# Kernel tuning notes

Hardware: AMD Instinct MI355X
Metric: run time of the kernel (lower is better)

The kernel has to match this reference:

```python
import jax, jax.numpy as jnp
import numpy as np

HID = 128
NEG = 9000000000000000.0  # 9e15 additive mask constant from the source


def setup_inputs() -> dict:
    key = jax.random.key(0)
    ks = jax.random.split(key, 20)
    B, N, OBS, N1, N2 = 32, 2048, 256, 8, 8
    x = jax.random.normal(ks[0], (B, N, OBS), dtype=jnp.float32)
    mask = jax.random.randint(ks[1], (B, N, N), 0, 2).astype(jnp.float32)

    def lin(kw, kb, fan_in, fan_out):
        bound = 1.0 / np.sqrt(fan_in)
        W = jax.random.uniform(kw, (fan_in, fan_out), jnp.float32, -bound, bound)
        b = jax.random.uniform(kb, (fan_out,), jnp.float32, -bound, bound)
        return W, b

    Wv, bv = lin(ks[2], ks[3], OBS, HID)
    Wk, bk = lin(ks[4], ks[5], OBS, HID)
    Wq, bq = lin(ks[6], ks[7], OBS, HID)
    Wout, bout = lin(ks[8], ks[9], HID, HID)
    Wval, bval = lin(ks[10], ks[11], HID, 1)
    Wadv1, badv1 = lin(ks[12], ks[13], HID, N1)
    Wadv2, badv2 = lin(ks[14], ks[15], HID, N2)
    return {
        'x': x, 'mask': mask,
        'Wv': Wv, 'bv': bv, 'Wk': Wk, 'bk': bk, 'Wq': Wq, 'bq': bq,
        'Wout': Wout, 'bout': bout, 'Wval': Wval, 'bval': bval,
        'Wadv1': Wadv1, 'badv1': badv1, 'Wadv2': Wadv2, 'badv2': badv2,
    }


def reference(x, mask, Wv, bv, Wk, bk, Wq, bq, Wout, bout,
              Wval, bval, Wadv1, badv1, Wadv2, badv2):
    # AttenModel
    v = jax.nn.relu(x @ Wv + bv)          # [B,N,H]
    q = jax.nn.relu(x @ Wq + bq)          # [B,N,H]
    k = jax.nn.relu(x @ Wk + bk)          # [B,N,H]
    scores = jnp.einsum('bnh,bmh->bnm', q, k)          # [B,N,N]
    scores = scores * mask - NEG * (1.0 - mask)
    att = jax.nn.softmax(scores, axis=2)
    out = jnp.einsum('bnm,bmh->bnh', att, v)            # [B,N,H]
    out = jax.nn.relu(out @ Wout + bout)                # [B,N,H]
    # Dueling heads (batch > 1, so squeeze(0) is a no-op)
    value = out @ Wval + bval                            # [B,N,1]
    adv1 = out @ Wadv1 + badv1                           # [B,N,n1]
    adv2 = out @ Wadv2 + badv2                           # [B,N,n2]
    q1 = value + adv1 - adv1.mean(axis=1, keepdims=True)
    q2 = value + adv2 - adv2.mean(axis=1, keepdims=True)
    return (q1, q2)
```

## Files before the change

kernel.cpp:

```cpp
#include <hip/hip_runtime.h>
#include <hip/hip_bf16.h>


typedef __attribute__((ext_vector_type(4))) float f32x4;
typedef __attribute__((ext_vector_type(8))) short bf16x8;
typedef __attribute__((ext_vector_type(4))) unsigned int u32x4;

#define LOG2E 1.44269504088896340736f
#define NEGC 9.0e15f

static __device__ __forceinline__ unsigned short f2bf(float f) {
  unsigned int x = __builtin_bit_cast(unsigned int, f);
  unsigned int r = (x + 0x7fffu + ((x >> 16) & 1u)) >> 16;
  return (unsigned short)r;
}
static __device__ __forceinline__ float bf2f(unsigned short u) {
  return __builtin_bit_cast(float, ((unsigned int)u) << 16);
}
static __device__ __forceinline__ unsigned int cvt_pk_bf16(float lo, float hi) {
  unsigned int r;
  asm("v_cvt_pk_bf16_f32 %0, %1, %2" : "=v"(r) : "v"(lo), "v"(hi));
  return r;
}
static __device__ __forceinline__ f32x4 mfma16(bf16x8 a, bf16x8 b, f32x4 c) {
  return __builtin_amdgcn_mfma_f32_16x16x32_bf16(a, b, c, 0, 0, 0);
}

__global__ __launch_bounds__(256) void prepack_kernel(
    const float* __restrict__ mask, unsigned long long* __restrict__ bits,
    const float* __restrict__ Wv, const float* __restrict__ Wk,
    const float* __restrict__ Wq, const float* __restrict__ Wout,
    unsigned short* __restrict__ Wf_hi, unsigned short* __restrict__ Wf_lo,
    unsigned short* __restrict__ WoutT) {
  if (blockIdx.x >= 2048) {
    int gid = (blockIdx.x - 2048) * 256 + threadIdx.x;
    if (gid < 12288) {
      int kc = gid / 1536;
      int rem = gid - kc * 1536;
      int t = rem >> 6, lane = rem & 63;
      int hf = lane & 15, qf = lane >> 4;
      int sec = t >> 3;
      int j = (t & 7) * 16 + hf;
      const float* W = (sec == 0) ? Wq : (sec == 1) ? Wk : Wv;
#pragma unroll
      for (int e = 0; e < 8; ++e) {
        int k = kc * 32 + qf * 8 + e;
        float w = W[k * 128 + j];
        unsigned short hi = f2bf(w);
        Wf_hi[gid * 8 + e] = hi;
        Wf_lo[gid * 8 + e] = f2bf(w - bf2f(hi));
      }
    } else if (gid < 12288 + 16384) {
      int i2 = gid - 12288;
      int j = i2 >> 7, c = i2 & 127;
      WoutT[i2] = f2bf(Wout[c * 128 + j]);
    }
    return;
  }
  const int lane = threadIdx.x & 63;
  const int gwave = (blockIdx.x << 2) | (threadIdx.x >> 6);
  const int T = lane & 3;
  const int sh = T << 4;
  for (int r = 0; r < 8; ++r) {
    const long row = (long)gwave * 8 + r;
    const float* mp = mask + row * 2048;
    unsigned long long* op = bits + row * 32;
#pragma unroll
    for (int g = 0; g < 8; ++g) {
      f32x4 v = *(const f32x4*)(mp + g * 256 + lane * 4);
      unsigned long long b0 = __ballot(v[0] != 0.0f);
      unsigned long long b1 = __ballot(v[1] != 0.0f);
      unsigned long long b2 = __ballot(v[2] != 0.0f);
      unsigned long long b3 = __ballot(v[3] != 0.0f);
      unsigned long long f0 = (b0 >> sh) & 0xFFFFull;
      unsigned long long f1 = (b1 >> sh) & 0xFFFFull;
      unsigned long long f2 = (b2 >> sh) & 0xFFFFull;
      unsigned long long f3 = (b3 >> sh) & 0xFFFFull;
      unsigned long long val = f0 | (f1 << 16) | (f2 << 32) | (f3 << 48);
      if (lane < 4) op[g * 4 + T] = val;
    }
  }
}

__global__ __launch_bounds__(256, 2) void proj_kernel(
    const float* __restrict__ x,
    const unsigned short* __restrict__ Wf_hi, const unsigned short* __restrict__ Wf_lo,
    const float* __restrict__ bq, const float* __restrict__ bk, const float* __restrict__ bv,
    unsigned short* __restrict__ q_bf, unsigned short* __restrict__ Kf,
    unsigned short* __restrict__ Vf) {
  __shared__ bf16x8 wst_hi[1536];
  __shared__ bf16x8 wst_lo[1536];
  __shared__ unsigned short vbuf[9216];

  const int tid = threadIdx.x;
  const int lane = tid & 63, wid = tid >> 6;
  const long rbase = (long)blockIdx.x * 64;
  const int qq = lane >> 4, hh = lane & 15;
  const long rowA = rbase + wid * 16 + hh;
  const f32x4 zero4 = {0.f, 0.f, 0.f, 0.f};
  f32x4 acc[24];
#pragma unroll
  for (int t = 0; t < 24; ++t) acc[t] = zero4;

  for (int kc = 0; kc < 8; ++kc) {
    __syncthreads();
#pragma unroll
    for (int i = 0; i < 6; ++i) {
      int idx = i * 256 + tid;
      wst_hi[idx] = *(const bf16x8*)(Wf_hi + ((long)kc * 1536 + idx) * 8);
      wst_lo[idx] = *(const bf16x8*)(Wf_lo + ((long)kc * 1536 + idx) * 8);
    }
    __syncthreads();

    const float* xp = x + rowA * 256 + kc * 32 + qq * 8;
    f32x4 x0 = *(const f32x4*)xp;
    f32x4 x1 = *(const f32x4*)(xp + 4);
    bf16x8 ah, al;
#pragma unroll
    for (int j = 0; j < 8; ++j) {
      float f = (j < 4) ? x0[j] : x1[j - 4];
      unsigned short h = f2bf(f);
      ah[j] = (short)h;
      al[j] = (short)f2bf(f - bf2f(h));
    }
#pragma unroll
    for (int t = 0; t < 24; ++t) {
      bf16x8 bh = wst_hi[t * 64 + lane];
      bf16x8 bl = wst_lo[t * 64 + lane];
      acc[t] = mfma16(ah, bh, acc[t]);
      acc[t] = mfma16(al, bh, acc[t]);
      acc[t] = mfma16(ah, bl, acc[t]);
    }
  }

  const int rowL = wid * 16 + qq * 4;
  const int b = (int)(rbase >> 11);
  const int tbase = (int)((rbase & 2047) >> 6);

  for (int sec = 0; sec < 3; ++sec) {
    __syncthreads();
#pragma unroll
    for (int tp = 0; tp < 8; ++tp) {
      const int t = sec * 8 + tp;
      const int j = tp * 16 + hh;
      const float bias = (sec == 0) ? bq[j] : (sec == 1) ? bk[j] : bv[j];
#pragma unroll
      for (int r = 0; r < 4; ++r) {
        unsigned short h = f2bf(fmaxf(acc[t][r] + bias, 0.f));
        if (sec == 2) vbuf[j * 72 + rowL + r] = h;
        else          vbuf[(rowL + r) * 136 + j] = h;
      }
    }
    __syncthreads();
    if (sec == 0) {
      const int row = tid >> 2, ch = tid & 3;
      bf16x8 w1 = *(const bf16x8*)&vbuf[row * 136 + ch * 32];
      bf16x8 w2 = *(const bf16x8*)&vbuf[row * 136 + ch * 32 + 8];
      bf16x8 w3 = *(const bf16x8*)&vbuf[row * 136 + ch * 32 + 16];
      bf16x8 w4 = *(const bf16x8*)&vbuf[row * 136 + ch * 32 + 24];
      unsigned short* op = q_bf + (rbase + row) * 128 + ch * 32;
      *(bf16x8*)op = w1;
      *(bf16x8*)(op + 8) = w2;
      *(bf16x8*)(op + 16) = w3;
      *(bf16x8*)(op + 24) = w4;
    } else if (sec == 1) {
#pragma unroll
      for (int it = 0; it < 4; ++it) {
        int gid = it * 256 + tid;
        int seg = gid >> 6, ln = gid & 63;
        int m = seg >> 2, kc = seg & 3;
        int hf = ln & 15, qf = ln >> 4;
        bf16x8 w = *(const bf16x8*)&vbuf[(m * 16 + hf) * 136 + kc * 32 + qf * 8];
        long off = (((long)(b * 32 + tbase) * 16 + seg) * 64 + ln) * 8;
        *(bf16x8*)(Kf + off) = w;
      }
    } else {
#pragma unroll
      for (int it = 0; it < 4; ++it) {
        int gid = it * 256 + tid;
        int seg = gid >> 6, ln = gid & 63;
        int ht = seg >> 1, c = seg & 1;
        int hf = ln & 15, qf = ln >> 4;
        bf16x8 w = *(const bf16x8*)&vbuf[(ht * 16 + hf) * 72 + c * 32 + qf * 8];
        long off = (((long)(b * 32 + tbase) * 16 + seg) * 64 + ln) * 8;
        *(bf16x8*)(Vf + off) = w;
      }
    }
  }
}

__global__ __launch_bounds__(256, 2) void attn_kernel(
    const unsigned short* __restrict__ q_bf, const unsigned short* __restrict__ Kf,
    const unsigned short* __restrict__ Vf,
    const unsigned long long* __restrict__ bits, unsigned short* __restrict__ out_att) {
  __shared__ bf16x8 kls[2][1024];
  __shared__ bf16x8 vls[2][1024];

  const int tid = threadIdx.x;
  const int lane = tid & 63, wid = tid >> 6;
  const int qq = lane >> 4, hh = lane & 15;
  const int orig = blockIdx.x;
  const int b = ((orig & 7) << 2) | ((orig >> 3) & 3);
  const int nb = orig >> 5;
  const long qbase = (long)b * 2048 + nb * 128 + wid * 32;

  const f32x4 zero4 = {0.f, 0.f, 0.f, 0.f};

  bf16x8 qh[2][4];
#pragma unroll
  for (int ctq = 0; ctq < 2; ++ctq)
#pragma unroll
    for (int kc = 0; kc < 4; ++kc)
      qh[ctq][kc] = *(const bf16x8*)(q_bf + (qbase + ctq * 16 + hh) * 128 + kc * 32 + qq * 8);

  const unsigned long long* br0 = bits + (qbase + hh) * 32;
  const unsigned long long* br1 = bits + (qbase + 16 + hh) * 32;
  const unsigned short* kf0 = Kf + (long)(b * 32) * 8192;
  const unsigned short* vf0 = Vf + (long)(b * 32) * 8192;

  f32x4 o_acc[8][2];
#pragma unroll
  for (int ht = 0; ht < 8; ++ht) { o_acc[ht][0] = zero4; o_acc[ht][1] = zero4; }
  float m_run[2] = {-3.0e38f, -3.0e38f};
  float l_run[2] = {0.f, 0.f};

  bf16x8 stg[8];
  const int seg0 = wid * 8;
  auto LOADREG = [&](int t) {
#pragma unroll
    for (int i = 0; i < 8; ++i) {
      int seg = seg0 + i;
      const unsigned short* src = (seg < 16)
          ? kf0 + (long)t * 8192 + (seg * 64 + lane) * 8
          : vf0 + (long)t * 8192 + ((seg - 16) * 64 + lane) * 8;
      stg[i] = *(const bf16x8*)src;
    }
  };
  auto WRITEBUF = [&](int nb2) {
#pragma unroll
    for (int i = 0; i < 8; ++i) {
      int seg = seg0 + i;
      if (seg < 16) kls[nb2][seg * 64 + lane] = stg[i];
      else          vls[nb2][(seg - 16) * 64 + lane] = stg[i];
    }
  };

  LOADREG(0);
  WRITEBUF(0);
  LOADREG(1);
  __syncthreads();

  unsigned long long bc0 = br0[0];
  unsigned long long bc1 = br1[0];
  int cur = 0;

  for (int t = 0; t < 32; ++t) {
    unsigned long long bn0 = 0, bn1 = 0;
    if (t + 1 < 32) { bn0 = br0[t + 1]; bn1 = br1[t + 1]; }

    if (t + 1 < 32) WRITEBUF(cur ^ 1);
    if (t + 2 < 32) LOADREG(t + 2);

    f32x4 s[2][4];
#pragma unroll
    for (int m = 0; m < 4; ++m) { s[0][m] = zero4; s[1][m] = zero4; }
    __builtin_amdgcn_s_setprio(1);
#pragma unroll
    for (int m = 0; m < 4; ++m) {
      bf16x8 khf[4];
#pragma unroll
      for (int kc = 0; kc < 4; ++kc) khf[kc] = kls[cur][(m * 4 + kc) * 64 + lane];
#pragma unroll
      for (int kc = 0; kc < 4; ++kc)
#pragma unroll
        for (int ctq = 0; ctq < 2; ++ctq)
          s[ctq][m] = mfma16(khf[kc], qh[ctq][kc], s[ctq][m]);
    }
    __builtin_amdgcn_s_setprio(0);

    {
      const unsigned long long bb0 = bc0 >> qq;
      const unsigned long long bb1 = bc1 >> qq;
#pragma unroll
      for (int m = 0; m < 4; ++m)
#pragma unroll
        for (int r = 0; r < 4; ++r) {
          const int sh = r * 16 + m * 4;
          s[0][m][r] = ((bb0 >> sh) & 1ull) ? s[0][m][r] : -NEGC;
          s[1][m][r] = ((bb1 >> sh) & 1ull) ? s[1][m][r] : -NEGC;
        }
    }

    unsigned int pk[2][4][2];
#pragma unroll
    for (int ctq = 0; ctq < 2; ++ctq) {
      float mx = s[ctq][0][0];
#pragma unroll
      for (int m = 0; m < 4; ++m)
#pragma unroll
        for (int r = 0; r < 4; ++r) mx = fmaxf(mx, s[ctq][m][r]);
      mx = fmaxf(mx, __shfl_xor(mx, 16, 64));
      mx = fmaxf(mx, __shfl_xor(mx, 32, 64));
      if (__any(mx > m_run[ctq] + 8.0f)) {
        float mnew = fmaxf(m_run[ctq], mx);
        float sc = exp2f((m_run[ctq] - mnew) * LOG2E);
        m_run[ctq] = mnew;
        l_run[ctq] *= sc;
#pragma unroll
        for (int ht = 0; ht < 8; ++ht) o_acc[ht][ctq] *= sc;
      }
      float ps = 0.f;
#pragma unroll
      for (int m = 0; m < 4; ++m)
#pragma unroll
        for (int r = 0; r < 4; ++r) {
          float p = exp2f((s[ctq][m][r] - m_run[ctq]) * LOG2E);
          s[ctq][m][r] = p;
          ps += p;
        }
      ps += __shfl_xor(ps, 16, 64);
      ps += __shfl_xor(ps, 32, 64);
      l_run[ctq] += ps;
#pragma unroll
      for (int m = 0; m < 4; ++m) {
        pk[ctq][m][0] = cvt_pk_bf16(s[ctq][m][0], s[ctq][m][1]);
        pk[ctq][m][1] = cvt_pk_bf16(s[ctq][m][2], s[ctq][m][3]);
      }
    }

    bf16x8 pb[2][2];
#pragma unroll
    for (int ctq = 0; ctq < 2; ++ctq)
#pragma unroll
      for (int c = 0; c < 2; ++c) {
        unsigned int a  = pk[ctq][2 * c][0];
        unsigned int bb = pk[ctq][2 * c][1];
        unsigned int cc = pk[ctq][2 * c + 1][0];
        unsigned int d  = pk[ctq][2 * c + 1][1];
        asm("v_permlane32_swap_b32 %0, %1" : "+v"(a),  "+v"(cc));
        asm("v_permlane32_swap_b32 %0, %1" : "+v"(bb), "+v"(d));
        asm("v_permlane16_swap_b32 %0, %1" : "+v"(a),  "+v"(cc));
        asm("v_permlane16_swap_b32 %0, %1" : "+v"(bb), "+v"(d));
        u32x4 w;
        w[0] = a; w[1] = bb; w[2] = cc; w[3] = d;
        pb[ctq][c] = __builtin_bit_cast(bf16x8, w);
      }

    __builtin_amdgcn_s_setprio(1);
#pragma unroll
    for (int ht = 0; ht < 8; ++ht)
#pragma unroll
      for (int c = 0; c < 2; ++c) {
        bf16x8 vf = vls[cur][(ht * 2 + c) * 64 + lane];
#pragma unroll
        for (int ctq = 0; ctq < 2; ++ctq)
          o_acc[ht][ctq] = mfma16(vf, pb[ctq][c], o_acc[ht][ctq]);
      }
    __builtin_amdgcn_s_setprio(0);

    __syncthreads();
    cur ^= 1;
    bc0 = bn0;
    bc1 = bn1;
  }

#pragma unroll
  for (int ctq = 0; ctq < 2; ++ctq) {
    float inv = 1.0f / l_run[ctq];
    const long row = qbase + ctq * 16 + hh;
#pragma unroll
    for (int ht = 0; ht < 8; ++ht) {
      f32x4 o = o_acc[ht][ctq];
      uint2 w;
      w.x = cvt_pk_bf16(o[0] * inv, o[1] * inv);
      w.y = cvt_pk_bf16(o[2] * inv, o[3] * inv);
      *(uint2*)(out_att + row * 128 + ht * 16 + qq * 4) = w;
    }
  }
}

__global__ __launch_bounds__(256) void wout_heads_kernel(
    const unsigned short* __restrict__ out_att, const unsigned short* __restrict__ WoutT,
    const float* __restrict__ bout,
    const float* __restrict__ Wval, const float* __restrict__ bval,
    const float* __restrict__ Wadv1, const float* __restrict__ badv1,
    const float* __restrict__ Wadv2, const float* __restrict__ badv2,
    float* __restrict__ value, float* __restrict__ adv1, float* __restrict__ adv2) {
  const int lane = threadIdx.x & 63, wid = threadIdx.x >> 6;
  const int qq = lane >> 4, hh = lane & 15;
  const long rowA = (long)blockIdx.x * 64 + wid * 16 + hh;
  const f32x4 zero4 = {0.f, 0.f, 0.f, 0.f};
  f32x4 acc[8];
#pragma unroll
  for (int t = 0; t < 8; ++t) acc[t] = zero4;
#pragma unroll
  for (int kc = 0; kc < 4; ++kc) {
    bf16x8 af = *(const bf16x8*)(out_att + rowA * 128 + kc * 32 + qq * 8);
#pragma unroll
    for (int t = 0; t < 8; ++t) {
      bf16x8 bf = *(const bf16x8*)(WoutT + (t * 16 + hh) * 128 + kc * 32 + qq * 8);
      acc[t] = mfma16(af, bf, acc[t]);
    }
  }
  float pv[4] = {0.f, 0.f, 0.f, 0.f};
  float pa1[4][8], pa2[4][8];
#pragma unroll
  for (int r = 0; r < 4; ++r)
#pragma unroll
    for (int j = 0; j < 8; ++j) { pa1[r][j] = 0.f; pa2[r][j] = 0.f; }
#pragma unroll
  for (int t = 0; t < 8; ++t) {
    const int col = t * 16 + hh;
    const float bo = bout[col];
    const float wv = Wval[col];
    const f32x4 w1a = *(const f32x4*)(Wadv1 + col * 8);
    const f32x4 w1b = *(const f32x4*)(Wadv1 + col * 8 + 4);
    const f32x4 w2a = *(const f32x4*)(Wadv2 + col * 8);
    const f32x4 w2b = *(const f32x4*)(Wadv2 + col * 8 + 4);
#pragma unroll
    for (int r = 0; r < 4; ++r) {
      float h = fmaxf(acc[t][r] + bo, 0.f);
      pv[r] += h * wv;
#pragma unroll
      for (int j = 0; j < 4; ++j) {
        pa1[r][j]     += h * w1a[j];
        pa1[r][4 + j] += h * w1b[j];
        pa2[r][j]     += h * w2a[j];
        pa2[r][4 + j] += h * w2b[j];
      }
    }
  }
#pragma unroll
  for (int r = 0; r < 4; ++r) {
#pragma unroll
    for (int s = 1; s < 16; s <<= 1) {
      pv[r] += __shfl_xor(pv[r], s, 64);
#pragma unroll
      for (int j = 0; j < 8; ++j) {
        pa1[r][j] += __shfl_xor(pa1[r][j], s, 64);
        pa2[r][j] += __shfl_xor(pa2[r][j], s, 64);
      }
    }
  }
  if (hh == 0) {
    const float bv0 = bval[0];
#pragma unroll
    for (int r = 0; r < 4; ++r) {
      const long row = (long)blockIdx.x * 64 + wid * 16 + qq * 4 + r;
      value[row] = pv[r] + bv0;
#pragma unroll
      for (int j = 0; j < 8; ++j) {
        adv1[row * 8 + j] = pa1[r][j] + badv1[j];
        adv2[row * 8 + j] = pa2[r][j] + badv2[j];
      }
    }
  }
}

__global__ __launch_bounds__(256) void combine_kernel(
    const float* __restrict__ value, const float* __restrict__ adv1,
    const float* __restrict__ adv2, float* __restrict__ out) {
  const int b = blockIdx.x >> 3;
  const int slice = blockIdx.x & 7;
  const int tid = threadIdx.x;
  __shared__ float red[4][16];

  float p[16];
#pragma unroll
  for (int j = 0; j < 16; ++j) p[j] = 0.f;
  for (int n = tid; n < 2048; n += 256) {
    const long row = (long)b * 2048 + n;
    const f32x4 a1a = *(const f32x4*)(adv1 + row * 8);
    const f32x4 a1b = *(const f32x4*)(adv1 + row * 8 + 4);
    const f32x4 a2a = *(const f32x4*)(adv2 + row * 8);
    const f32x4 a2b = *(const f32x4*)(adv2 + row * 8 + 4);
#pragma unroll
    for (int j = 0; j < 4; ++j) {
      p[j] += a1a[j]; p[4 + j] += a1b[j];
      p[8 + j] += a2a[j]; p[12 + j] += a2b[j];
    }
  }
#pragma unroll
  for (int s = 1; s < 64; s <<= 1)
#pragma unroll
    for (int j = 0; j < 16; ++j) p[j] += __shfl_xor(p[j], s, 64);
  const int wid = tid >> 6;
  if ((tid & 63) == 0)
#pragma unroll
    for (int j = 0; j < 16; ++j) red[wid][j] = p[j];
  __syncthreads();

  float mean1[8], mean2[8];
#pragma unroll
  for (int j = 0; j < 8; ++j) {
    mean1[j] = (red[0][j] + red[1][j] + red[2][j] + red[3][j]) * (1.0f / 2048.0f);
    mean2[j] = (red[0][8 + j] + red[1][8 + j] + red[2][8 + j] + red[3][8 + j]) * (1.0f / 2048.0f);
  }

  const int n = slice * 256 + tid;
  const long row = (long)b * 2048 + n;
  const float v = value[row];
  const f32x4 a1a = *(const f32x4*)(adv1 + row * 8);
  const f32x4 a1b = *(const f32x4*)(adv1 + row * 8 + 4);
  const f32x4 a2a = *(const f32x4*)(adv2 + row * 8);
  const f32x4 a2b = *(const f32x4*)(adv2 + row * 8 + 4);
  f32x4 o1a, o1b, o2a, o2b;
#pragma unroll
  for (int j = 0; j < 4; ++j) {
    o1a[j] = v + a1a[j] - mean1[j];
    o1b[j] = v + a1b[j] - mean1[4 + j];
    o2a[j] = v + a2a[j] - mean2[j];
    o2b[j] = v + a2b[j] - mean2[4 + j];
  }
  *(f32x4*)(out + row * 8) = o1a;
  *(f32x4*)(out + row * 8 + 4) = o1b;
  *(f32x4*)(out + 524288 + row * 8) = o2a;
  *(f32x4*)(out + 524288 + row * 8 + 4) = o2b;
}

extern "C" void kernel_launch(void* const* d_in, const int* in_sizes, int n_in,
                              void* d_out, int out_size, void* d_ws, size_t ws_size,
                              hipStream_t stream) {
  const float* x     = (const float*)d_in[0];
  const float* mask  = (const float*)d_in[1];
  const float* Wv    = (const float*)d_in[2];
  const float* bv    = (const float*)d_in[3];
  const float* Wk    = (const float*)d_in[4];
  const float* bk    = (const float*)d_in[5];
  const float* Wq    = (const float*)d_in[6];
  const float* bq    = (const float*)d_in[7];
  const float* Wout  = (const float*)d_in[8];
  const float* bout  = (const float*)d_in[9];
  const float* Wval  = (const float*)d_in[10];
  const float* bval  = (const float*)d_in[11];
  const float* Wadv1 = (const float*)d_in[12];
  const float* badv1 = (const float*)d_in[13];
  const float* Wadv2 = (const float*)d_in[14];
  const float* badv2 = (const float*)d_in[15];
  float* out = (float*)d_out;
  char* ws = (char*)d_ws;

  unsigned short* q_bf   = (unsigned short*)(ws + 0);
  unsigned short* Kf     = (unsigned short*)(ws + 16777216);
  unsigned short* Vf     = (unsigned short*)(ws + 33554432);
  unsigned short* out_at = (unsigned short*)(ws + 50331648);
  float* value = (float*)(ws + 67108864);
  float* adv1  = (float*)(ws + 67371008);
  float* adv2  = (float*)(ws + 69468160);
  unsigned short* Wf_hi = (unsigned short*)(ws + 71567360);
  unsigned short* Wf_lo = (unsigned short*)(ws + 71763968);
  unsigned short* WoutT = (unsigned short*)(ws + 71960576);
  unsigned long long* bits = (unsigned long long*)(ws + 71993344);

  prepack_kernel<<<2160, 256, 0, stream>>>(mask, bits, Wv, Wk, Wq, Wout,
                                           Wf_hi, Wf_lo, WoutT);
  proj_kernel<<<1024, 256, 0, stream>>>(x, Wf_hi, Wf_lo, bq, bk, bv, q_bf, Kf, Vf);
  attn_kernel<<<512, 256, 0, stream>>>(q_bf, Kf, Vf, bits, out_at);
  wout_heads_kernel<<<1024, 256, 0, stream>>>(out_at, WoutT, bout, Wval, bval,
                                              Wadv1, badv1, Wadv2, badv2,
                                              value, adv1, adv2);
  combine_kernel<<<256, 256, 0, stream>>>(value, adv1, adv2, out);
}
```

Baseline: 324.0 us.

## Double query rows per attention wave to halve K/V tile reloads

```diff
diff --git a/kernel.cpp b/kernel.cpp
--- a/kernel.cpp
+++ b/kernel.cpp
@@ -189,7 +189,7 @@
   }
 }
 
-__global__ __launch_bounds__(256, 2) void attn_kernel(
+__global__ __launch_bounds__(256, 1) void attn_kernel(
     const unsigned short* __restrict__ q_bf, const unsigned short* __restrict__ Kf,
     const unsigned short* __restrict__ Vf,
     const unsigned long long* __restrict__ bits, unsigned short* __restrict__ out_att) {
@@ -202,27 +202,31 @@
   const int orig = blockIdx.x;
   const int b = ((orig & 7) << 2) | ((orig >> 3) & 3);
   const int nb = orig >> 5;
-  const long qbase = (long)b * 2048 + nb * 128 + wid * 32;
+  const long qbase = (long)b * 2048 + nb * 256 + wid * 64;
 
   const f32x4 zero4 = {0.f, 0.f, 0.f, 0.f};
 
-  bf16x8 qh[2][4];
-#pragma unroll
-  for (int ctq = 0; ctq < 2; ++ctq)
+  bf16x8 qh[4][4];
+#pragma unroll
+  for (int ctq = 0; ctq < 4; ++ctq)
 #pragma unroll
     for (int kc = 0; kc < 4; ++kc)
       qh[ctq][kc] = *(const bf16x8*)(q_bf + (qbase + ctq * 16 + hh) * 128 + kc * 32 + qq * 8);
 
-  const unsigned long long* br0 = bits + (qbase + hh) * 32;
-  const unsigned long long* br1 = bits + (qbase + 16 + hh) * 32;
+  const unsigned long long* br[4];
+#pragma unroll
+  for (int ctq = 0; ctq < 4; ++ctq)
+    br[ctq] = bits + (qbase + ctq * 16 + hh) * 32;
   const unsigned short* kf0 = Kf + (long)(b * 32) * 8192;
   const unsigned short* vf0 = Vf + (long)(b * 32) * 8192;
 
-  f32x4 o_acc[8][2];
-#pragma unroll
-  for (int ht = 0; ht < 8; ++ht) { o_acc[ht][0] = zero4; o_acc[ht][1] = zero4; }
-  float m_run[2] = {-3.0e38f, -3.0e38f};
-  float l_run[2] = {0.f, 0.f};
+  f32x4 o_acc[8][4];
+#pragma unroll
+  for (int ht = 0; ht < 8; ++ht)
+#pragma unroll
+    for (int ctq = 0; ctq < 4; ++ctq) o_acc[ht][ctq] = zero4;
+  float m_run[4] = {-3.0e38f, -3.0e38f, -3.0e38f, -3.0e38f};
+  float l_run[4] = {0.f, 0.f, 0.f, 0.f};
 
   bf16x8 stg[8];
   const int seg0 = wid * 8;
@@ -250,20 +254,24 @@
   LOADREG(1);
   __syncthreads();
 
-  unsigned long long bc0 = br0[0];
-  unsigned long long bc1 = br1[0];
+  unsigned long long bc[4], bn[4];
+#pragma unroll
+  for (int ctq = 0; ctq < 4; ++ctq) bc[ctq] = br[ctq][0];
   int cur = 0;
 
   for (int t = 0; t < 32; ++t) {
-    unsigned long long bn0 = 0, bn1 = 0;
-    if (t + 1 < 32) { bn0 = br0[t + 1]; bn1 = br1[t + 1]; }
+#pragma unroll
+    for (int ctq = 0; ctq < 4; ++ctq)
+      bn[ctq] = (t + 1 < 32) ? br[ctq][t + 1] : 0;
 
     if (t + 1 < 32) WRITEBUF(cur ^ 1);
     if (t + 2 < 32) LOADREG(t + 2);
 
-    f32x4 s[2][4];
-#pragma unroll
-    for (int m = 0; m < 4; ++m) { s[0][m] = zero4; s[1][m] = zero4; }
+    f32x4 s[4][4];
+#pragma unroll
+    for (int ctq = 0; ctq < 4; ++ctq)
+#pragma unroll
+      for (int m = 0; m < 4; ++m) s[ctq][m] = zero4;
     __builtin_amdgcn_s_setprio(1);
 #pragma unroll
     for (int m = 0; m < 4; ++m) {
@@ -273,27 +281,26 @@
 #pragma unroll
       for (int kc = 0; kc < 4; ++kc)
 #pragma unroll
-        for (int ctq = 0; ctq < 2; ++ctq)
+        for (int ctq = 0; ctq < 4; ++ctq)
           s[ctq][m] = mfma16(khf[kc], qh[ctq][kc], s[ctq][m]);
     }
     __builtin_amdgcn_s_setprio(0);
 
-    {
-      const unsigned long long bb0 = bc0 >> qq;
-      const unsigned long long bb1 = bc1 >> qq;
+#pragma unroll
+    for (int ctq = 0; ctq < 4; ++ctq) {
+      const unsigned long long bb = bc[ctq] >> qq;
 #pragma unroll
       for (int m = 0; m < 4; ++m)
 #pragma unroll
         for (int r = 0; r < 4; ++r) {
           const int sh = r * 16 + m * 4;
-          s[0][m][r] = ((bb0 >> sh) & 1ull) ? s[0][m][r] : -NEGC;
-          s[1][m][r] = ((bb1 >> sh) & 1ull) ? s[1][m][r] : -NEGC;
+          s[ctq][m][r] = ((bb >> sh) & 1ull) ? s[ctq][m][r] : -NEGC;
         }
     }
 
-    unsigned int pk[2][4][2];
-#pragma unroll
-    for (int ctq = 0; ctq < 2; ++ctq) {
+    unsigned int pk[4][4][2];
+#pragma unroll
+    for (int ctq = 0; ctq < 4; ++ctq) {
       float mx = s[ctq][0][0];
 #pragma unroll
       for (int m = 0; m < 4; ++m)
@@ -328,9 +335,9 @@
       }
     }
 
-    bf16x8 pb[2][2];
-#pragma unroll
-    for (int ctq = 0; ctq < 2; ++ctq)
+    bf16x8 pb[4][2];
+#pragma unroll
+    for (int ctq = 0; ctq < 4; ++ctq)
 #pragma unroll
       for (int c = 0; c < 2; ++c) {
         unsigned int a  = pk[ctq][2 * c][0];
@@ -353,19 +360,19 @@
       for (int c = 0; c < 2; ++c) {
         bf16x8 vf = vls[cur][(ht * 2 + c) * 64 + lane];
 #pragma unroll
-        for (int ctq = 0; ctq < 2; ++ctq)
+        for (int ctq = 0; ctq < 4; ++ctq)
           o_acc[ht][ctq] = mfma16(vf, pb[ctq][c], o_acc[ht][ctq]);
       }
     __builtin_amdgcn_s_setprio(0);
 
     __syncthreads();
     cur ^= 1;
-    bc0 = bn0;
-    bc1 = bn1;
-  }
-
-#pragma unroll
-  for (int ctq = 0; ctq < 2; ++ctq) {
+#pragma unroll
+    for (int ctq = 0; ctq < 4; ++ctq) bc[ctq] = bn[ctq];
+  }
+
+#pragma unroll
+  for (int ctq = 0; ctq < 4; ++ctq) {
     float inv = 1.0f / l_run[ctq];
     const long row = qbase + ctq * 16 + hh;
 #pragma unroll
@@ -555,7 +562,7 @@
   prepack_kernel<<<2160, 256, 0, stream>>>(mask, bits, Wv, Wk, Wq, Wout,
                                            Wf_hi, Wf_lo, WoutT);
   proj_kernel<<<1024, 256, 0, stream>>>(x, Wf_hi, Wf_lo, bq, bk, bv, q_bf, Kf, Vf);
-  attn_kernel<<<512, 256, 0, stream>>>(q_bf, Kf, Vf, bits, out_at);
+  attn_kernel<<<256, 256, 0, stream>>>(q_bf, Kf, Vf, bits, out_at);
   wout_heads_kernel<<<1024, 256, 0, stream>>>(out_at, WoutT, bout, Wval, bval,
                                               Wadv1, badv1, Wadv2, badv2,
                                               value, adv1, adv2);
```

Result: slower. 376.3 us (+16.1%).
